# Kernel optimization log

Measured on AMD Instinct MI355X. Metric: run time of the kernel, lower is better.

The kernel has to match this reference:

```python
import jax, jax.numpy as jnp
import numpy as np
from jax import lax

EPS = 1e-08


def setup_inputs() -> dict:
    key = jax.random.key(0)
    k1, k2, k3, k4 = jax.random.split(key, 4)
    b, cin, cout, hw, kk = 32, 256, 256, 64, 3
    fan_in = cin * kk * kk
    # kaiming_normal_(a=0, mode='fan_in', nonlinearity='leaky_relu') -> gain=sqrt(2), std=sqrt(2/fan_in)
    w_std = np.sqrt(2.0 / fan_in).astype(np.float32)
    return {
        "x": jax.random.normal(k1, (b, cin, hw, hw), dtype=jnp.float32),
        "y": jax.random.normal(k2, (b, cin), dtype=jnp.float32),
        "weight": jax.random.normal(k3, (cout, cin, kk, kk), dtype=jnp.float32) * w_std,
        "bias": jax.random.normal(k4, (cout,), dtype=jnp.float32) * 0.1,
    }


def _modulated_conv(x, y, weight, bias):
    # x: [b, cin, h, w]; y: [b, cin]; weight: [cout, cin, kh, kw]; bias: [cout]
    # modulate: per-sample scale of input channels
    w = weight[None] * (y[:, None, :, None, None] + 1.0)  # [b, cout, cin, kh, kw]
    # demodulate: normalize each (sample, out-channel) filter
    d = lax.rsqrt(jnp.sum(w * w, axis=(2, 3, 4), keepdims=True) + EPS)
    w = w * d

    def conv_one(xi, wi):
        # xi: [cin, h, w]; wi: [cout, cin, kh, kw]
        out = lax.conv_general_dilated(
            xi[None], wi, window_strides=(1, 1), padding="SAME",
            dimension_numbers=("NCHW", "OIHW", "NCHW"))
        return out[0]  # [cout, h, w]

    out = jax.vmap(conv_one)(x, w)  # [b, cout, h, w]
    return out + bias[None, :, None, None]


def reference(x, y, weight, bias):
    return _modulated_conv(x, y, weight, bias)
```

## Files before the change

### kernel.cpp

```cpp
#include <hip/hip_runtime.h>
#include <hip/hip_bf16.h>

typedef __attribute__((ext_vector_type(8))) short short8;
typedef __attribute__((ext_vector_type(4))) float f32x4;

#define XT_IMG_BYTES (66*66*256*2)
#define XT_TOTAL_BYTES (32LL*XT_IMG_BYTES)
#define WM_ROW_BYTES (2304*2)
#define WM_IMG_BYTES (256*WM_ROW_BYTES)

static __device__ __forceinline__ void async16(void* lds, const void* g) {
  __builtin_amdgcn_global_load_lds((const __attribute__((address_space(1))) void*)g,
                                   (__attribute__((address_space(3))) void*)lds, 16, 0, 0);
}
static __device__ __forceinline__ ushort f2bf(float f) {
  __hip_bfloat16 h = __float2bfloat16(f);
  return *reinterpret_cast<ushort*>(&h);
}

__global__ __launch_bounds__(256) void k_prep(const float* __restrict__ x,
                                              const float* __restrict__ W,
                                              const float* __restrict__ y,
                                              ushort* __restrict__ xT,
                                              ushort* __restrict__ wmod) {
  __shared__ float smem[64][65];
  const int bid = blockIdx.x;
  const int t   = threadIdx.x;

  if (bid < 8192) {
    const int b  = bid >> 8;
    const int h  = (bid >> 2) & 63;
    const int c0 = (bid & 3) << 6;
    const int tw = t & 63, tg = t >> 6;
    const float* xp = x + (size_t)(b * 256 + c0) * 4096 + h * 64 + tw;
#pragma unroll
    for (int j = 0; j < 16; ++j) {
      int il = j * 4 + tg;
      smem[il][tw] = xp[(size_t)il * 4096];
    }
    __syncthreads();
    const int q  = t & 7;
    const int w0 = t >> 3;
    ushort* op = xT + (size_t)b * (66 * 66 * 256) + ((size_t)(h + 1) * 66 + 1) * 256 + c0;
#pragma unroll
    for (int j = 0; j < 2; ++j) {
      const int wl = j * 32 + w0;
      short8 v;
#pragma unroll
      for (int k2 = 0; k2 < 8; ++k2) v[k2] = (short)f2bf(smem[8 * q + k2][wl]);
      *(short8*)(op + (size_t)wl * 256 + 8 * q) = v;
    }
  } else if (bid < 16384) {
    float* red = &smem[0][0];
    const int bb = bid - 8192;
    const int b = bb >> 8, o = bb & 255;
    const float* wp = W + (size_t)(o * 256 + t) * 9;
    float wr[9];
#pragma unroll
    for (int r = 0; r < 9; ++r) wr[r] = wp[r];
    const float ym = y[b * 256 + t] + 1.0f;
    float ss = 0.f;
#pragma unroll
    for (int r = 0; r < 9; ++r) ss += wr[r] * wr[r];
    red[t] = ss * ym * ym;
    __syncthreads();
    for (int s = 128; s > 0; s >>= 1) {
      if (t < s) red[t] += red[t + s];
      __syncthreads();
    }
    const float sc = rsqrtf(red[0] + 1e-8f) * ym;
    ushort* op = wmod + (size_t)(b * 256 + o) * 2304 + t;
#pragma unroll
    for (int r = 0; r < 9; ++r) op[r * 256] = f2bf(wr[r] * sc);
  } else {
    const int zb = bid - 16384;
    const int b  = zb >> 3;
    const int tt = ((zb & 7) << 8) | t;
    uint4* xT4 = (uint4*)xT;
    const uint4 z = make_uint4(0u, 0u, 0u, 0u);
    uint4* base = xT4 + (size_t)b * (66 * 66 * 32);
    uint4* r0  = base;
    uint4* r65 = base + (size_t)65 * 66 * 32;
    for (int i = tt; i < 2112; i += 2048) { r0[i] = z; r65[i] = z; }
    {
      int r = (tt >> 5) + 1, c = tt & 31;
      base[((size_t)r * 66 + 0)  * 32 + c] = z;
      base[((size_t)r * 66 + 65) * 32 + c] = z;
    }
  }
}

__global__ __launch_bounds__(512, 2) void k_gemm(const ushort* __restrict__ wmod,
                                                 const ushort* __restrict__ xT,
                                                 const float* __restrict__ bias,
                                                 float* __restrict__ out) {
  __shared__ ushort ldsA[2][16384];
  __shared__ ushort ldsB[2][16384];

  const int t  = threadIdx.x;
  const int bx = blockIdx.x;
  const int xcd = bx & 7;
  const int idx = bx >> 3;
  const int b   = xcd + ((idx >> 4) << 3);
  const int tn  = idx & 15;
  const int n0  = tn << 8;
  const int h0  = tn << 2;

  const int ln = t & 15;
  const int kq = (t >> 4) & 3;
  const int wv = t >> 6;
  const int wm = wv >> 2;
  const int wn = wv & 3;

  const char* wmodB = (const char*)wmod + (size_t)b * WM_IMG_BYTES;
  const char* xTB   = (const char*)xT   + (size_t)b * XT_IMG_BYTES;

  int gAoff[4], gBoff[4];
#pragma unroll
  for (int j = 0; j < 4; ++j) {
    const int s = j * 512 + t;
    const int row = s >> 3, g = s & 7;
    gAoff[j] = row * WM_ROW_BYTES + ((g ^ (row & 7)) << 4);
    const int hr = row >> 6, wc = row & 63;
    gBoff[j] = ((h0 + hr) * 66 + wc) * 512 + ((g ^ (row & 7)) << 4);
  }

  const int swz = ln & 7;
  const int g0 = ((0 | kq) ^ swz) << 3;
  const int g1 = ((4 | kq) ^ swz) << 3;
  const int aBase = (wm * 128 + ln) * 64;
  const int bBase = (wn * 64  + ln) * 64;

  f32x4 acc[8][4];
  const f32x4 z4 = {0.f, 0.f, 0.f, 0.f};
#pragma unroll
  for (int i = 0; i < 8; ++i)
#pragma unroll
    for (int j = 0; j < 4; ++j) acc[i][j] = z4;

#define LOAD_A(J, KO, BUF) async16(&ldsA[BUF][0] + ((J) * 512 + t) * 8, wmodB + gAoff[J] + (KO))
#define LOAD_B(J, KO, BUF) async16(&ldsB[BUF][0] + ((J) * 512 + t) * 8, xTB   + gBoff[J] + (KO))

#define MF(F, E, A, B) acc[F][E] = __builtin_amdgcn_mfma_f32_16x16x32_bf16(A, B, acc[F][E], 0, 0, 0)
#define FENCE() __builtin_amdgcn_sched_barrier(0)
#define BAR()   __builtin_amdgcn_s_barrier()

  LOAD_A(0, 0, 0); LOAD_A(1, 0, 0); LOAD_A(2, 0, 0); LOAD_A(3, 0, 0);
  LOAD_B(0, 0, 0); LOAD_B(1, 0, 0); LOAD_B(2, 0, 0); LOAD_B(3, 0, 0);
  {
    const int koA1 = 0 * 512 + 128;
    const int koB1 = (0 * 66 + 0) * 512 + 128;
    LOAD_A(0, koA1, 1); LOAD_A(2, koA1, 1);
    LOAD_B(0, koB1, 1); LOAD_B(1, koB1, 1); LOAD_B(2, koB1, 1); LOAD_B(3, koB1, 1);
  }
  asm volatile("s_waitcnt vmcnt(6)" ::: "memory");
  FENCE(); BAR(); FENCE();

#pragma unroll 1
  for (int kt = 0; kt < 36; ++kt) {
    const int cur = kt & 1, nb = cur ^ 1;
    const ushort* bufA = &ldsA[cur][0];
    const ushort* bufB = &ldsB[cur][0];

    const int n1 = kt + 1;
    const int koA1 = (n1 >> 2) * 512 + ((n1 & 3) << 7);
    const int n2 = kt + 2;
    const int r2 = n2 >> 2;
    const int kh2 = r2 / 3, kw2 = r2 - kh2 * 3;
    const int koA2 = r2 * 512 + ((n2 & 3) << 7);
    const int koB2 = (kh2 * 66 + kw2) * 512 + ((n2 & 3) << 7);

    short8 A0 = *(const short8*)(bufA + aBase + 0 * 1024 + g0);
    short8 A1 = *(const short8*)(bufA + aBase + 1 * 1024 + g0);
    short8 A2 = *(const short8*)(bufA + aBase + 2 * 1024 + g0);
    short8 A3 = *(const short8*)(bufA + aBase + 3 * 1024 + g0);
    short8 B0 = *(const short8*)(bufB + bBase + 0 * 1024 + g0);
    short8 B1 = *(const short8*)(bufB + bBase + 1 * 1024 + g0);
    short8 B2 = *(const short8*)(bufB + bBase + 2 * 1024 + g0);
    short8 B3 = *(const short8*)(bufB + bBase + 3 * 1024 + g0);
    if (kt < 35) { LOAD_A(1, koA1, nb); LOAD_A(3, koA1, nb); }
    __builtin_amdgcn_s_setprio(1);
    MF(0,0,A0,B0); MF(1,0,A1,B0); MF(2,0,A2,B0); MF(3,0,A3,B0);
    MF(0,1,A0,B1); MF(1,1,A1,B1); MF(2,1,A2,B1); MF(3,1,A3,B1);
    MF(0,2,A0,B2); MF(1,2,A1,B2); MF(2,2,A2,B2); MF(3,2,A3,B2);
    MF(0,3,A0,B3); MF(1,3,A1,B3); MF(2,3,A2,B3); MF(3,3,A3,B3);
    __builtin_amdgcn_s_setprio(0);

    short8 A4 = *(const short8*)(bufA + aBase + 4 * 1024 + g0);
    short8 A5 = *(const short8*)(bufA + aBase + 5 * 1024 + g0);
    short8 A6 = *(const short8*)(bufA + aBase + 6 * 1024 + g0);
    short8 A7 = *(const short8*)(bufA + aBase + 7 * 1024 + g0);
    __builtin_amdgcn_s_setprio(1);
    MF(4,0,A4,B0); MF(5,0,A5,B0); MF(6,0,A6,B0); MF(7,0,A7,B0);
    MF(4,1,A4,B1); MF(5,1,A5,B1); MF(6,1,A6,B1); MF(7,1,A7,B1);
    MF(4,2,A4,B2); MF(5,2,A5,B2); MF(6,2,A6,B2); MF(7,2,A7,B2);
    MF(4,3,A4,B3); MF(5,3,A5,B3); MF(6,3,A6,B3); MF(7,3,A7,B3);
    __builtin_amdgcn_s_setprio(0);
    FENCE();

    short8 C0 = *(const short8*)(bufA + aBase + 0 * 1024 + g1);
    short8 C1 = *(const short8*)(bufA + aBase + 1 * 1024 + g1);
    short8 C2 = *(const short8*)(bufA + aBase + 2 * 1024 + g1);
    short8 C3 = *(const short8*)(bufA + aBase + 3 * 1024 + g1);
    short8 D0 = *(const short8*)(bufB + bBase + 0 * 1024 + g1);
    short8 D1 = *(const short8*)(bufB + bBase + 1 * 1024 + g1);
    short8 D2 = *(const short8*)(bufB + bBase + 2 * 1024 + g1);
    short8 D3 = *(const short8*)(bufB + bBase + 3 * 1024 + g1);
    __builtin_amdgcn_s_setprio(1);
    MF(0,0,C0,D0); MF(1,0,C1,D0); MF(2,0,C2,D0); MF(3,0,C3,D0);
    MF(0,1,C0,D1); MF(1,1,C1,D1); MF(2,1,C2,D1); MF(3,1,C3,D1);
    MF(0,2,C0,D2); MF(1,2,C1,D2); MF(2,2,C2,D2); MF(3,2,C3,D2);
    MF(0,3,C0,D3); MF(1,3,C1,D3); MF(2,3,C2,D3); MF(3,3,C3,D3);
    __builtin_amdgcn_s_setprio(0);

    FENCE(); BAR(); FENCE();

    short8 C4 = *(const short8*)(bufA + aBase + 4 * 1024 + g1);
    short8 C5 = *(const short8*)(bufA + aBase + 5 * 1024 + g1);
    short8 C6 = *(const short8*)(bufA + aBase + 6 * 1024 + g1);
    short8 C7 = *(const short8*)(bufA + aBase + 7 * 1024 + g1);
    if (kt < 34) {
      LOAD_A(0, koA2, cur); LOAD_A(2, koA2, cur);
      LOAD_B(0, koB2, cur); LOAD_B(1, koB2, cur);
      LOAD_B(2, koB2, cur); LOAD_B(3, koB2, cur);
    }
    __builtin_amdgcn_s_setprio(1);
    MF(4,0,C4,D0); MF(5,0,C5,D0); MF(6,0,C6,D0); MF(7,0,C7,D0);
    MF(4,1,C4,D1); MF(5,1,C5,D1); MF(6,1,C6,D1); MF(7,1,C7,D1);
    MF(4,2,C4,D2); MF(5,2,C5,D2); MF(6,2,C6,D2); MF(7,2,C7,D2);
    MF(4,3,C4,D3); MF(5,3,C5,D3); MF(6,3,C6,D3); MF(7,3,C7,D3);
    __builtin_amdgcn_s_setprio(0);

    if (kt < 34) {
      asm volatile("s_waitcnt vmcnt(6)" ::: "memory");
    } else {
      asm volatile("s_waitcnt vmcnt(0)" ::: "memory");
    }
    FENCE(); BAR(); FENCE();
  }

  const float* bp = bias + wm * 128;
  float* outB = out + ((size_t)(b * 256 + wm * 128)) * 4096 + n0 + wn * 64 + ln;
#pragma unroll
  for (int mi = 0; mi < 8; ++mi) {
#pragma unroll
    for (int rg = 0; rg < 4; ++rg) {
      const int orow = mi * 16 + kq * 4 + rg;
      const float bv = bp[orow];
      float* po = outB + (size_t)orow * 4096;
#pragma unroll
      for (int ni = 0; ni < 4; ++ni) po[ni * 16] = acc[mi][ni][rg] + bv;
    }
  }
#undef LOAD_A
#undef LOAD_B
#undef MF
#undef FENCE
#undef BAR
}

extern "C" void kernel_launch(void* const* d_in, const int* in_sizes, int n_in,
                              void* d_out, int out_size, void* d_ws, size_t ws_size,
                              hipStream_t stream) {
  const float* x    = (const float*)d_in[0];
  const float* y    = (const float*)d_in[1];
  const float* W    = (const float*)d_in[2];
  const float* bias = (const float*)d_in[3];
  float* out = (float*)d_out;

  ushort* xT   = (ushort*)d_ws;
  ushort* wmod = (ushort*)((char*)d_ws + (size_t)XT_TOTAL_BYTES);

  k_prep<<<16640, 256, 0, stream>>>(x, W, y, xT, wmod);
  k_gemm<<<512,   512, 0, stream>>>(wmod, xT, bias, out);
}
```

Measured before the change: 373.8 us.

## Rebalance GEMM LDS prefetch schedule and vectorize prep transpose loads

The GEMM main loop now splits the B-tile global-to-LDS loads evenly between the two prefetch points: two B loads issue with the next stage's A loads and two with the stage-after-next, instead of all four at once. It also adds barrier-plus-lgkmcnt(0) fences around each MFMA cluster so waves interleave LDS reads and matrix ops in a ping-pong pattern. The prep kernel switches x reads to float4 loads with a padded 68-wide LDS tile. The extra barriers add synchronisation overhead, and the 68-float row stride may bring back bank conflicts in the transposing reads.

```diff
diff --git a/kernel.cpp b/kernel.cpp
--- a/kernel.cpp
+++ b/kernel.cpp
@@ -23,7 +23,7 @@
                                               const float* __restrict__ y,
                                               ushort* __restrict__ xT,
                                               ushort* __restrict__ wmod) {
-  __shared__ float smem[64][65];
+  __shared__ float smem[64][68];
   const int bid = blockIdx.x;
   const int t   = threadIdx.x;
 
@@ -31,12 +31,12 @@
     const int b  = bid >> 8;
     const int h  = (bid >> 2) & 63;
     const int c0 = (bid & 3) << 6;
-    const int tw = t & 63, tg = t >> 6;
-    const float* xp = x + (size_t)(b * 256 + c0) * 4096 + h * 64 + tw;
-#pragma unroll
-    for (int j = 0; j < 16; ++j) {
-      int il = j * 4 + tg;
-      smem[il][tw] = xp[(size_t)il * 4096];
+    const float* xp = x + (size_t)(b * 256 + c0) * 4096 + h * 64;
+#pragma unroll
+    for (int j = 0; j < 4; ++j) {
+      const int lin = j * 1024 + t * 4;
+      const int il = lin >> 6, c = lin & 63;
+      *(float4*)&smem[il][c] = *(const float4*)(xp + (size_t)il * 4096 + c);
     }
     __syncthreads();
     const int q  = t & 7;
@@ -144,26 +144,26 @@
 #define MF(F, E, A, B) acc[F][E] = __builtin_amdgcn_mfma_f32_16x16x32_bf16(A, B, acc[F][E], 0, 0, 0)
 #define FENCE() __builtin_amdgcn_sched_barrier(0)
 #define BAR()   __builtin_amdgcn_s_barrier()
+#define LGKM0() do { asm volatile("s_waitcnt lgkmcnt(0)" ::: "memory"); FENCE(); } while (0)
 
   LOAD_A(0, 0, 0); LOAD_A(1, 0, 0); LOAD_A(2, 0, 0); LOAD_A(3, 0, 0);
   LOAD_B(0, 0, 0); LOAD_B(1, 0, 0); LOAD_B(2, 0, 0); LOAD_B(3, 0, 0);
-  {
-    const int koA1 = 0 * 512 + 128;
-    const int koB1 = (0 * 66 + 0) * 512 + 128;
-    LOAD_A(0, koA1, 1); LOAD_A(2, koA1, 1);
-    LOAD_B(0, koB1, 1); LOAD_B(1, koB1, 1); LOAD_B(2, koB1, 1); LOAD_B(3, koB1, 1);
-  }
-  asm volatile("s_waitcnt vmcnt(6)" ::: "memory");
-  FENCE(); BAR(); FENCE();
+  LOAD_A(0, 128, 1); LOAD_A(2, 128, 1);
+  LOAD_B(0, 128, 1); LOAD_B(1, 128, 1);
+  asm volatile("s_waitcnt vmcnt(4)" ::: "memory");
+  FENCE(); BAR();
 
 #pragma unroll 1
   for (int kt = 0; kt < 36; ++kt) {
-    const int cur = kt & 1, nb = cur ^ 1;
-    const ushort* bufA = &ldsA[cur][0];
-    const ushort* bufB = &ldsB[cur][0];
+    const int s = kt & 1, sn = s ^ 1;
+    const ushort* bufA = &ldsA[s][0];
+    const ushort* bufB = &ldsB[s][0];
 
     const int n1 = kt + 1;
-    const int koA1 = (n1 >> 2) * 512 + ((n1 & 3) << 7);
+    const int r1 = n1 >> 2;
+    const int kh1 = r1 / 3, kw1 = r1 - kh1 * 3;
+    const int koA1 = r1 * 512 + ((n1 & 3) << 7);
+    const int koB1 = (kh1 * 66 + kw1) * 512 + ((n1 & 3) << 7);
     const int n2 = kt + 2;
     const int r2 = n2 >> 2;
     const int kh2 = r2 / 3, kw2 = r2 - kh2 * 3;
@@ -178,25 +178,31 @@
     short8 B1 = *(const short8*)(bufB + bBase + 1 * 1024 + g0);
     short8 B2 = *(const short8*)(bufB + bBase + 2 * 1024 + g0);
     short8 B3 = *(const short8*)(bufB + bBase + 3 * 1024 + g0);
-    if (kt < 35) { LOAD_A(1, koA1, nb); LOAD_A(3, koA1, nb); }
+    if (kt < 35) {
+      LOAD_A(1, koA1, sn); LOAD_A(3, koA1, sn);
+      LOAD_B(2, koB1, sn); LOAD_B(3, koB1, sn);
+    }
+    BAR(); LGKM0();
     __builtin_amdgcn_s_setprio(1);
     MF(0,0,A0,B0); MF(1,0,A1,B0); MF(2,0,A2,B0); MF(3,0,A3,B0);
     MF(0,1,A0,B1); MF(1,1,A1,B1); MF(2,1,A2,B1); MF(3,1,A3,B1);
     MF(0,2,A0,B2); MF(1,2,A1,B2); MF(2,2,A2,B2); MF(3,2,A3,B2);
     MF(0,3,A0,B3); MF(1,3,A1,B3); MF(2,3,A2,B3); MF(3,3,A3,B3);
     __builtin_amdgcn_s_setprio(0);
+    FENCE(); BAR();
 
     short8 A4 = *(const short8*)(bufA + aBase + 4 * 1024 + g0);
     short8 A5 = *(const short8*)(bufA + aBase + 5 * 1024 + g0);
     short8 A6 = *(const short8*)(bufA + aBase + 6 * 1024 + g0);
     short8 A7 = *(const short8*)(bufA + aBase + 7 * 1024 + g0);
+    BAR(); LGKM0();
     __builtin_amdgcn_s_setprio(1);
     MF(4,0,A4,B0); MF(5,0,A5,B0); MF(6,0,A6,B0); MF(7,0,A7,B0);
     MF(4,1,A4,B1); MF(5,1,A5,B1); MF(6,1,A6,B1); MF(7,1,A7,B1);
     MF(4,2,A4,B2); MF(5,2,A5,B2); MF(6,2,A6,B2); MF(7,2,A7,B2);
     MF(4,3,A4,B3); MF(5,3,A5,B3); MF(6,3,A6,B3); MF(7,3,A7,B3);
     __builtin_amdgcn_s_setprio(0);
-    FENCE();
+    FENCE(); BAR();
 
     short8 C0 = *(const short8*)(bufA + aBase + 0 * 1024 + g1);
     short8 C1 = *(const short8*)(bufA + aBase + 1 * 1024 + g1);
@@ -206,37 +212,37 @@
     short8 D1 = *(const short8*)(bufB + bBase + 1 * 1024 + g1);
     short8 D2 = *(const short8*)(bufB + bBase + 2 * 1024 + g1);
     short8 D3 = *(const short8*)(bufB + bBase + 3 * 1024 + g1);
+    BAR(); LGKM0();
     __builtin_amdgcn_s_setprio(1);
     MF(0,0,C0,D0); MF(1,0,C1,D0); MF(2,0,C2,D0); MF(3,0,C3,D0);
     MF(0,1,C0,D1); MF(1,1,C1,D1); MF(2,1,C2,D1); MF(3,1,C3,D1);
     MF(0,2,C0,D2); MF(1,2,C1,D2); MF(2,2,C2,D2); MF(3,2,C3,D2);
     MF(0,3,C0,D3); MF(1,3,C1,D3); MF(2,3,C2,D3); MF(3,3,C3,D3);
     __builtin_amdgcn_s_setprio(0);
-
-    FENCE(); BAR(); FENCE();
+    FENCE(); BAR();
 
     short8 C4 = *(const short8*)(bufA + aBase + 4 * 1024 + g1);
     short8 C5 = *(const short8*)(bufA + aBase + 5 * 1024 + g1);
     short8 C6 = *(const short8*)(bufA + aBase + 6 * 1024 + g1);
     short8 C7 = *(const short8*)(bufA + aBase + 7 * 1024 + g1);
     if (kt < 34) {
-      LOAD_A(0, koA2, cur); LOAD_A(2, koA2, cur);
-      LOAD_B(0, koB2, cur); LOAD_B(1, koB2, cur);
-      LOAD_B(2, koB2, cur); LOAD_B(3, koB2, cur);
-    }
+      LOAD_A(0, koA2, s); LOAD_A(2, koA2, s);
+      LOAD_B(0, koB2, s); LOAD_B(1, koB2, s);
+    }
+    BAR(); LGKM0();
     __builtin_amdgcn_s_setprio(1);
     MF(4,0,C4,D0); MF(5,0,C5,D0); MF(6,0,C6,D0); MF(7,0,C7,D0);
     MF(4,1,C4,D1); MF(5,1,C5,D1); MF(6,1,C6,D1); MF(7,1,C7,D1);
     MF(4,2,C4,D2); MF(5,2,C5,D2); MF(6,2,C6,D2); MF(7,2,C7,D2);
     MF(4,3,C4,D3); MF(5,3,C5,D3); MF(6,3,C6,D3); MF(7,3,C7,D3);
     __builtin_amdgcn_s_setprio(0);
-
+    FENCE();
     if (kt < 34) {
-      asm volatile("s_waitcnt vmcnt(6)" ::: "memory");
+      asm volatile("s_waitcnt vmcnt(4)" ::: "memory");
     } else {
       asm volatile("s_waitcnt vmcnt(0)" ::: "memory");
     }
-    FENCE(); BAR(); FENCE();
+    FENCE(); BAR();
   }
 
   const float* bp = bias + wm * 128;
@@ -257,6 +263,7 @@
 #undef MF
 #undef FENCE
 #undef BAR
+#undef LGKM0
 }
 
 extern "C" void kernel_launch(void* const* d_in, const int* in_sizes, int n_in,
```

Measured after the change: 383.6 us. 2.6% more time.
